# Optimization experiments

Measured on AMD Instinct MI355X. Metric: run time of the kernel, lower is better.

The kernel has to match this reference:

```python
import jax, jax.numpy as jnp
import numpy as np

KERNEL_MUL = 2.0
KERNEL_NUM = 5
SIZE = 128  # hardcoded slice size in the original forward


def setup_inputs() -> dict:
    key = jax.random.key(0)
    k1, k2 = jax.random.split(key)
    B, D, S = 64, 4096, 128
    source = jax.random.normal(k1, (B, D, S), dtype=jnp.float32)
    target = jax.random.normal(k2, (B, D, S), dtype=jnp.float32)
    return {"source": source, "target": target}


def _mmd_rbf(source, target):
    # source/target: [B, D, S] with S == SIZE
    B, D, S = source.shape
    # per-sample: permute to [S, D] and concat -> total: [B, 2S, D]
    x = jnp.concatenate(
        [jnp.transpose(source, (0, 2, 1)), jnp.transpose(target, (0, 2, 1))], axis=1
    )
    n = 2 * S
    sq = jnp.sum(x * x, axis=-1)  # [B, 2S]
    # pairwise squared L2 via Gram matrix (avoids [2S,2S,D] expansion)
    gram = jnp.einsum("bnd,bmd->bnm", x, x)  # [B, 2S, 2S]
    L2 = sq[:, :, None] + sq[:, None, :] - 2.0 * gram  # [B, 2S, 2S]
    # bandwidth from detached distances (torch uses L2_distance.data)
    bw = jax.lax.stop_gradient(jnp.sum(L2, axis=(1, 2))) / (n * n - n)  # [B]
    bw = bw / (KERNEL_MUL ** (KERNEL_NUM // 2))
    scales = KERNEL_MUL ** jnp.arange(KERNEL_NUM, dtype=jnp.float32)  # [K]
    bws = bw[:, None, None, None] * scales[None, :, None, None]  # [B, K, 1, 1]
    kernels = jnp.sum(jnp.exp(-L2[:, None, :, :] / bws), axis=1)  # [B, 2S, 2S]
    K = jnp.mean(kernels, axis=0)  # sum over batch / B -> [2S, 2S]
    loss = (
        jnp.mean(K[:SIZE, :SIZE])
        + jnp.mean(K[SIZE:, SIZE:])
        - jnp.mean(K[:SIZE, SIZE:])
        - jnp.mean(K[SIZE:, :SIZE])
    )
    return loss


def reference(source, target):
    return _mmd_rbf(source, target)
```

## Files before the change

### kernel.cpp

```cpp
#include <hip/hip_runtime.h>

#define B_  64
#define D_  4096
#define S_  128
#define N_  256
#define KC_ 4
#define KPB (D_ / KC_)
#define BK  32
#define NCH (KPB / BK)
#define RS  40
#define LDSBUF (N_ * RS)
#define TILE_ (N_ * N_)

using short8   = __attribute__((ext_vector_type(8)))  short;
using floatx16 = __attribute__((ext_vector_type(16))) float;

__device__ __forceinline__ unsigned int f2bf(float f) {
  unsigned int u = __builtin_bit_cast(unsigned int, f);
  return (u + 0x7FFFu + ((u >> 16) & 1u)) >> 16;
}

__device__ __forceinline__ int swz(int n, int g) {
  return n * RS + (((g ^ (n & 3) ^ ((n >> 3) & 3)) & 3) << 3);
}

__global__ __launch_bounds__(512, 4) void k_gram(
    const float* __restrict__ src, const float* __restrict__ tgt,
    float* __restrict__ partial, float* __restrict__ tot,
    float* __restrict__ sq) {
  __shared__ unsigned short lds[2 * LDSBUF];
  __shared__ float red[8];
  const int bx  = blockIdx.x;
  const int kc  = bx >> 1;
  const int rh  = bx & 1;
  const int b   = blockIdx.y;
  const int tid = threadIdx.x;
  const int l   = tid & 63;
  const int w   = tid >> 6;
  const int tr  = w >> 2;
  const int tc  = w & 3;

  const int n_s = tid & 255;
  const int g   = tid >> 8;
  const float* colbase = (n_s < S_)
      ? (src + (size_t)b * D_ * S_ + n_s)
      : (tgt + (size_t)b * D_ * S_ + (n_s - S_));
  const float* pA = colbase + (size_t)kc * KPB * S_;

  float ld[16];
  floatx16 acc[2][2];
  #pragma unroll
  for (int i = 0; i < 2; i++)
    #pragma unroll
    for (int j = 0; j < 2; j++)
      #pragma unroll
      for (int r = 0; r < 16; r++) acc[i][j][r] = 0.f;

  const int lm   = l & 31;
  const int lk   = l >> 5;
  const int ar   = rh * 128 + tr * 64 + lm;
  const int bcol = tc * 64 + lm;

  #define LOADCH(ch)                                                   \
    do {                                                               \
      const float* q = pA + (size_t)(ch) * BK * S_;                    \
      _Pragma("unroll")                                                \
      for (int j = 0; j < 8; j++) {                                    \
        ld[j]     = q[(size_t)(g * 8 + j) * S_];                       \
        ld[8 + j] = q[(size_t)((g + 2) * 8 + j) * S_];                 \
      }                                                                \
    } while (0)

  #define WRITECH(buf)                                                 \
    do {                                                               \
      uint4 wa, wb;                                                    \
      wa.x = f2bf(ld[0])  | (f2bf(ld[1])  << 16);                      \
      wa.y = f2bf(ld[2])  | (f2bf(ld[3])  << 16);                      \
      wa.z = f2bf(ld[4])  | (f2bf(ld[5])  << 16);                      \
      wa.w = f2bf(ld[6])  | (f2bf(ld[7])  << 16);                      \
      wb.x = f2bf(ld[8])  | (f2bf(ld[9])  << 16);                      \
      wb.y = f2bf(ld[10]) | (f2bf(ld[11]) << 16);                      \
      wb.z = f2bf(ld[12]) | (f2bf(ld[13]) << 16);                      \
      wb.w = f2bf(ld[14]) | (f2bf(ld[15]) << 16);                      \
      const int base = (buf) * LDSBUF;                                 \
      *(uint4*)&lds[base + swz(n_s, g)]     = wa;                      \
      *(uint4*)&lds[base + swz(n_s, g + 2)] = wb;                      \
    } while (0)

  #define MFMACH(buf)                                                  \
    do {                                                               \
      const unsigned short* L = &lds[(buf) * LDSBUF];                  \
      _Pragma("unroll")                                                \
      for (int ks = 0; ks < 2; ks++) {                                 \
        const int gg = ks * 2 + lk;                                    \
        short8 a0 = *(const short8*)&L[swz(ar,        gg)];            \
        short8 a1 = *(const short8*)&L[swz(ar + 32,   gg)];            \
        short8 b0 = *(const short8*)&L[swz(bcol,      gg)];            \
        short8 b1 = *(const short8*)&L[swz(bcol + 32, gg)];            \
        acc[0][0] = __builtin_amdgcn_mfma_f32_32x32x16_bf16(a0, b0, acc[0][0], 0, 0, 0); \
        acc[0][1] = __builtin_amdgcn_mfma_f32_32x32x16_bf16(a0, b1, acc[0][1], 0, 0, 0); \
        acc[1][0] = __builtin_amdgcn_mfma_f32_32x32x16_bf16(a1, b0, acc[1][0], 0, 0, 0); \
        acc[1][1] = __builtin_amdgcn_mfma_f32_32x32x16_bf16(a1, b1, acc[1][1], 0, 0, 0); \
      }                                                                \
    } while (0)

  LOADCH(0);
  WRITECH(0);
  __syncthreads();
  for (int ch = 0; ch < NCH - 1; ch++) {
    LOADCH(ch + 1);
    MFMACH(ch & 1);
    WRITECH((ch + 1) & 1);
    __syncthreads();
  }
  MFMACH((NCH - 1) & 1);

  float* gb = partial + ((size_t)kc * B_ + b) * TILE_;
  #pragma unroll
  for (int i = 0; i < 2; i++)
    #pragma unroll
    for (int j = 0; j < 2; j++)
      #pragma unroll
      for (int r = 0; r < 16; r++) {
        const int row = (r & 3) + 8 * (r >> 2) + 4 * lk;
        const int nr  = rh * 128 + tr * 64 + i * 32 + row;
        const int nc  = tc * 64 + j * 32 + (l & 31);
        gb[nr * N_ + nc] = acc[i][j][r];
      }

  float s = 0.f;
  #pragma unroll
  for (int i = 0; i < 2; i++)
    #pragma unroll
    for (int j = 0; j < 2; j++)
      #pragma unroll
      for (int r = 0; r < 16; r++) s += acc[i][j][r];
  for (int off = 32; off; off >>= 1) s += __shfl_down(s, off);
  if (l == 0) red[w] = s;
  __syncthreads();
  if (tid == 0) {
    float T = red[0] + red[1] + red[2] + red[3]
            + red[4] + red[5] + red[6] + red[7];
    atomicAdd(&tot[b], T);
  }

  if ((rh * 2 + tr) == tc && lk == ((l >> 2) & 1)) {
    const int c = l & 31;
    const int r = (c >> 3) * 4 + (c & 3);
    #pragma unroll
    for (int i = 0; i < 2; i++)
      atomicAdd(&sq[b * N_ + tc * 64 + i * 32 + c], acc[i][i][r]);
  }
  #undef LOADCH
  #undef WRITECH
  #undef MFMACH
}

__global__ __launch_bounds__(1024, 2) void k_exp(
    const float* __restrict__ partial, const float* __restrict__ tot,
    const float* __restrict__ sq, float* __restrict__ out) {
  __shared__ float sqs[N_];
  __shared__ float red[16];
  __shared__ float bws;
  const int rc = blockIdx.x & 3;
  const int b  = blockIdx.x >> 2;
  const int t  = threadIdx.x;
  const int c  = t & 255;
  const int sg = t >> 8;

  if (t < N_) sqs[t] = sq[b * N_ + t];
  __syncthreads();
  if (t < N_) {
    float v = sqs[t];
    for (int off = 32; off; off >>= 1) v += __shfl_down(v, off);
    if ((t & 63) == 0) red[t >> 6] = v;
  }
  __syncthreads();
  if (t == 0) {
    float ssq = red[0] + red[1] + red[2] + red[3];
    float SL2 = 2.f * (float)N_ * ssq - 2.f * tot[b];
    bws = SL2 / (float)(N_ * N_ - N_) * 0.25f;
  }
  __syncthreads();

  const float bwv = bws;
  float nb[5];
  #pragma unroll
  for (int k = 0; k < 5; k++)
    nb[k] = -1.4426950408889634f / (bwv * (float)(1 << k));
  const float sqc = sqs[c];
  const float sgn = ((rc < 2) == (c < S_)) ? 1.f : -1.f;

  const float* p0 = partial + (size_t)b * TILE_;
  float accv = 0.f;
  #pragma unroll 4
  for (int i = 0; i < 16; i++) {
    const int row = rc * 64 + sg * 16 + i;
    float gg = p0[row * N_ + c]
             + p0[(size_t)1 * B_ * TILE_ + row * N_ + c]
             + p0[(size_t)2 * B_ * TILE_ + row * N_ + c]
             + p0[(size_t)3 * B_ * TILE_ + row * N_ + c];
    const float L2 = sqs[row] + sqc - 2.f * gg;
    float s = 0.f;
    #pragma unroll
    for (int k = 0; k < 5; k++) s += exp2f(L2 * nb[k]);
    accv += s;
  }
  accv *= sgn;
  for (int off = 32; off; off >>= 1) accv += __shfl_down(accv, off);
  __syncthreads();
  if ((t & 63) == 0) red[t >> 6] = accv;
  __syncthreads();
  if (t == 0) {
    float s = 0.f;
    #pragma unroll
    for (int i = 0; i < 16; i++) s += red[i];
    atomicAdd(out, s * (1.0f / (64.f * 16384.f)));
  }
}

extern "C" void kernel_launch(void* const* d_in, const int* in_sizes, int n_in,
                              void* d_out, int out_size, void* d_ws, size_t ws_size,
                              hipStream_t stream) {
  const float* src = (const float*)d_in[0];
  const float* tgt = (const float*)d_in[1];
  const size_t partial_bytes = (size_t)KC_ * B_ * TILE_ * sizeof(float);
  float* partial = (float*)d_ws;
  float* tot     = (float*)((char*)d_ws + partial_bytes);
  float* sq      = tot + B_;
  hipMemsetAsync(tot, 0, (B_ + B_ * N_) * sizeof(float), stream);
  hipMemsetAsync(d_out, 0, sizeof(float), stream);
  k_gram<<<dim3(KC_ * 2, B_), 512, 0, stream>>>(src, tgt, partial, tot, sq);
  k_exp<<<4 * B_, 1024, 0, stream>>>(partial, tot, sq, (float*)d_out);
}
```

Baseline: 310.8 us.

## Double k-chunk depth, use hardware bf16 pack, vectorize exp kernel loads

The gram kernel now stages 64-wide k chunks instead of 32, issuing loads and LDS writes in two halves that interleave with MFMA work, which halves the number of barriers per block. The software float-to-bf16 rounding is replaced by the v_cvt_pk_bf16_f32 instruction. The exp kernel moves to a 2D grid of 512-thread blocks and reads the four partial Gram slices with float4 loads. The larger LDS buffers per block may reduce occupancy, and the hardware conversion instruction must round the same way as the old software routine.

```diff
diff --git a/kernel.cpp b/kernel.cpp
--- a/kernel.cpp
+++ b/kernel.cpp
@@ -6,22 +6,23 @@
 #define N_  256
 #define KC_ 4
 #define KPB (D_ / KC_)
-#define BK  32
+#define BK  64
 #define NCH (KPB / BK)
-#define RS  40
+#define RS  72
 #define LDSBUF (N_ * RS)
 #define TILE_ (N_ * N_)
 
 using short8   = __attribute__((ext_vector_type(8)))  short;
 using floatx16 = __attribute__((ext_vector_type(16))) float;
 
-__device__ __forceinline__ unsigned int f2bf(float f) {
-  unsigned int u = __builtin_bit_cast(unsigned int, f);
-  return (u + 0x7FFFu + ((u >> 16) & 1u)) >> 16;
+__device__ __forceinline__ unsigned int pk2(float lo, float hi) {
+  unsigned int r;
+  asm("v_cvt_pk_bf16_f32 %0, %1, %2" : "=v"(r) : "v"(lo), "v"(hi));
+  return r;
 }
 
 __device__ __forceinline__ int swz(int n, int g) {
-  return n * RS + (((g ^ (n & 3) ^ ((n >> 3) & 3)) & 3) << 3);
+  return n * RS + ((g ^ (n & 3) ^ ((n >> 3) & 3)) << 3);
 }
 
 __global__ __launch_bounds__(512, 4) void k_gram(
@@ -61,37 +62,37 @@
   const int ar   = rh * 128 + tr * 64 + lm;
   const int bcol = tc * 64 + lm;
 
-  #define LOADCH(ch)                                                   \
+  #define LOADH(ch, gb)                                                \
     do {                                                               \
       const float* q = pA + (size_t)(ch) * BK * S_;                    \
       _Pragma("unroll")                                                \
       for (int j = 0; j < 8; j++) {                                    \
-        ld[j]     = q[(size_t)(g * 8 + j) * S_];                       \
-        ld[8 + j] = q[(size_t)((g + 2) * 8 + j) * S_];                 \
+        ld[j]     = q[(size_t)(((gb)) * 8 + j) * S_];                  \
+        ld[8 + j] = q[(size_t)(((gb) + 2) * 8 + j) * S_];              \
       }                                                                \
     } while (0)
 
-  #define WRITECH(buf)                                                 \
+  #define WRITEH(buf, gb)                                              \
     do {                                                               \
       uint4 wa, wb;                                                    \
-      wa.x = f2bf(ld[0])  | (f2bf(ld[1])  << 16);                      \
-      wa.y = f2bf(ld[2])  | (f2bf(ld[3])  << 16);                      \
-      wa.z = f2bf(ld[4])  | (f2bf(ld[5])  << 16);                      \
-      wa.w = f2bf(ld[6])  | (f2bf(ld[7])  << 16);                      \
-      wb.x = f2bf(ld[8])  | (f2bf(ld[9])  << 16);                      \
-      wb.y = f2bf(ld[10]) | (f2bf(ld[11]) << 16);                      \
-      wb.z = f2bf(ld[12]) | (f2bf(ld[13]) << 16);                      \
-      wb.w = f2bf(ld[14]) | (f2bf(ld[15]) << 16);                      \
-      const int base = (buf) * LDSBUF;                                 \
-      *(uint4*)&lds[base + swz(n_s, g)]     = wa;                      \
-      *(uint4*)&lds[base + swz(n_s, g + 2)] = wb;                      \
+      wa.x = pk2(ld[0],  ld[1]);                                       \
+      wa.y = pk2(ld[2],  ld[3]);                                       \
+      wa.z = pk2(ld[4],  ld[5]);                                       \
+      wa.w = pk2(ld[6],  ld[7]);                                       \
+      wb.x = pk2(ld[8],  ld[9]);                                       \
+      wb.y = pk2(ld[10], ld[11]);                                      \
+      wb.z = pk2(ld[12], ld[13]);                                      \
+      wb.w = pk2(ld[14], ld[15]);                                      \
+      const int base_ = (buf) * LDSBUF;                                \
+      *(uint4*)&lds[base_ + swz(n_s, (gb))]     = wa;                  \
+      *(uint4*)&lds[base_ + swz(n_s, (gb) + 2)] = wb;                  \
     } while (0)
 
-  #define MFMACH(buf)                                                  \
+  #define MFMA2(buf, k0)                                               \
     do {                                                               \
       const unsigned short* L = &lds[(buf) * LDSBUF];                  \
       _Pragma("unroll")                                                \
-      for (int ks = 0; ks < 2; ks++) {                                 \
+      for (int ks = (k0); ks < (k0) + 2; ks++) {                       \
         const int gg = ks * 2 + lk;                                    \
         short8 a0 = *(const short8*)&L[swz(ar,        gg)];            \
         short8 a1 = *(const short8*)&L[swz(ar + 32,   gg)];            \
@@ -104,16 +105,22 @@
       }                                                                \
     } while (0)
 
-  LOADCH(0);
-  WRITECH(0);
+  LOADH(0, g);
+  WRITEH(0, g);
+  LOADH(0, g + 4);
+  WRITEH(0, g + 4);
   __syncthreads();
   for (int ch = 0; ch < NCH - 1; ch++) {
-    LOADCH(ch + 1);
-    MFMACH(ch & 1);
-    WRITECH((ch + 1) & 1);
+    LOADH(ch + 1, g);
+    MFMA2(ch & 1, 0);
+    WRITEH((ch + 1) & 1, g);
+    LOADH(ch + 1, g + 4);
+    MFMA2(ch & 1, 2);
+    WRITEH((ch + 1) & 1, g + 4);
     __syncthreads();
   }
-  MFMACH((NCH - 1) & 1);
+  MFMA2((NCH - 1) & 1, 0);
+  MFMA2((NCH - 1) & 1, 2);
 
   float* gb = partial + ((size_t)kc * B_ + b) * TILE_;
   #pragma unroll
@@ -151,22 +158,22 @@
     for (int i = 0; i < 2; i++)
       atomicAdd(&sq[b * N_ + tc * 64 + i * 32 + c], acc[i][i][r]);
   }
-  #undef LOADCH
-  #undef WRITECH
-  #undef MFMACH
-}
-
-__global__ __launch_bounds__(1024, 2) void k_exp(
+  #undef LOADH
+  #undef WRITEH
+  #undef MFMA2
+}
+
+__global__ __launch_bounds__(512, 4) void k_exp(
     const float* __restrict__ partial, const float* __restrict__ tot,
     const float* __restrict__ sq, float* __restrict__ out) {
   __shared__ float sqs[N_];
-  __shared__ float red[16];
+  __shared__ float red[8];
   __shared__ float bws;
-  const int rc = blockIdx.x & 3;
-  const int b  = blockIdx.x >> 2;
+  const int rc = blockIdx.x;
+  const int b  = blockIdx.y;
   const int t  = threadIdx.x;
-  const int c  = t & 255;
-  const int sg = t >> 8;
+  const int cg = t & 63;
+  const int rg = t >> 6;
 
   if (t < N_) sqs[t] = sq[b * N_ + t];
   __syncthreads();
@@ -188,23 +195,31 @@
   #pragma unroll
   for (int k = 0; k < 5; k++)
     nb[k] = -1.4426950408889634f / (bwv * (float)(1 << k));
-  const float sqc = sqs[c];
-  const float sgn = ((rc < 2) == (c < S_)) ? 1.f : -1.f;
-
+
+  const int c4 = cg * 4;
+  const float4 sqc = *(const float4*)&sqs[c4];
+  const float sgn = ((rc < 4) == (cg < 32)) ? 1.f : -1.f;
   const float* p0 = partial + (size_t)b * TILE_;
+
   float accv = 0.f;
-  #pragma unroll 4
-  for (int i = 0; i < 16; i++) {
-    const int row = rc * 64 + sg * 16 + i;
-    float gg = p0[row * N_ + c]
-             + p0[(size_t)1 * B_ * TILE_ + row * N_ + c]
-             + p0[(size_t)2 * B_ * TILE_ + row * N_ + c]
-             + p0[(size_t)3 * B_ * TILE_ + row * N_ + c];
-    const float L2 = sqs[row] + sqc - 2.f * gg;
-    float s = 0.f;
-    #pragma unroll
-    for (int k = 0; k < 5; k++) s += exp2f(L2 * nb[k]);
-    accv += s;
+  #pragma unroll
+  for (int r = 0; r < 4; r++) {
+    const int row = rc * 32 + rg * 4 + r;
+    const float4 g0 = *(const float4*)&p0[row * N_ + c4];
+    const float4 g1 = *(const float4*)&p0[(size_t)1 * B_ * TILE_ + row * N_ + c4];
+    const float4 g2 = *(const float4*)&p0[(size_t)2 * B_ * TILE_ + row * N_ + c4];
+    const float4 g3 = *(const float4*)&p0[(size_t)3 * B_ * TILE_ + row * N_ + c4];
+    const float sr = sqs[row];
+    float4 L2;
+    L2.x = sr + sqc.x - 2.f * (g0.x + g1.x + g2.x + g3.x);
+    L2.y = sr + sqc.y - 2.f * (g0.y + g1.y + g2.y + g3.y);
+    L2.z = sr + sqc.z - 2.f * (g0.z + g1.z + g2.z + g3.z);
+    L2.w = sr + sqc.w - 2.f * (g0.w + g1.w + g2.w + g3.w);
+    #pragma unroll
+    for (int k = 0; k < 5; k++) {
+      accv += exp2f(L2.x * nb[k]) + exp2f(L2.y * nb[k])
+            + exp2f(L2.z * nb[k]) + exp2f(L2.w * nb[k]);
+    }
   }
   accv *= sgn;
   for (int off = 32; off; off >>= 1) accv += __shfl_down(accv, off);
@@ -212,10 +227,9 @@
   if ((t & 63) == 0) red[t >> 6] = accv;
   __syncthreads();
   if (t == 0) {
-    float s = 0.f;
-    #pragma unroll
-    for (int i = 0; i < 16; i++) s += red[i];
-    atomicAdd(out, s * (1.0f / (64.f * 16384.f)));
+    float s2 = red[0] + red[1] + red[2] + red[3]
+             + red[4] + red[5] + red[6] + red[7];
+    atomicAdd(out, s2 * (1.0f / (64.f * 16384.f)));
   }
 }
 
@@ -231,5 +245,5 @@
   hipMemsetAsync(tot, 0, (B_ + B_ * N_) * sizeof(float), stream);
   hipMemsetAsync(d_out, 0, sizeof(float), stream);
   k_gram<<<dim3(KC_ * 2, B_), 512, 0, stream>>>(src, tgt, partial, tot, sq);
-  k_exp<<<4 * B_, 1024, 0, stream>>>(partial, tot, sq, (float*)d_out);
-}
+  k_exp<<<dim3(8, B_), 512, 0, stream>>>(partial, tot, sq, (float*)d_out);
+}
```

Result: no change. 309.4 us (-0.5%).
